# Performance work log

Measured on AMD Instinct MI355X. Metric: run time of the kernel, lower is better.

## Reference

```python
import jax, jax.numpy as jnp
import numpy as np

N, E = 16384, 262144
IN, H, OUT = 128, 256, 256
L, HEADS = 4, 8
OC = H // HEADS  # 32, also MHA head_dim
B, NB = 64, 256  # graphs, nodes per graph (N = B*NB, equal-size graphs)


def _ln(x, g, b, eps=1e-5):
    m = x.mean(-1, keepdims=True)
    v = ((x - m) ** 2).mean(-1, keepdims=True)
    return (x - m) / jnp.sqrt(v + eps) * g + b


def setup_inputs() -> dict:
    key = jax.random.key(0)
    ks = iter(jax.random.split(key, 40))
    r = lambda *s: jax.random.normal(next(ks), s, jnp.float32) * 0.05
    return dict(
        x=jax.random.normal(next(ks), (N, IN), jnp.float32),
        edge_index=jax.random.randint(next(ks), (2, E), 0, N),
        wi=r(IN, H), bi=r(H),
        wg=r(L, H, H), asrc=r(L, HEADS, OC), adst=r(L, HEADS, OC), bg=r(L, H),
        g1=jnp.ones((L, H)), b1=jnp.zeros((L, H)),
        inw=r(L, 3 * H, H), inb=r(L, 3 * H), ow=r(L, H, H), ob=r(L, H),
        g2=jnp.ones((L, H)), b2=jnp.zeros((L, H)),
        mw1=r(L, H, 2 * H), mb1=r(L, 2 * H), mw2=r(L, 2 * H, H), mb2=r(L, H),
        g3=jnp.ones((L, H)), b3=jnp.zeros((L, H)),
        gf=jnp.ones(H), bf=jnp.zeros(H),
        wo=r(H, OUT), bo=r(OUT),
    )


def reference(x, edge_index, wi, bi, wg, asrc, adst, bg, g1, b1, inw, inb,
              ow, ob, g2, b2, mw1, mb1, mw2, mb2, g3, b3, gf, bf, wo, bo):
    src, dst = edge_index[0], edge_index[1]
    x = jax.nn.relu(x @ wi + bi)  # [N, H]
    for i in range(L):
        # ---- GATConv (local MPNN), eval mode (no dropout) ----
        xw = (x @ wg[i]).reshape(N, HEADS, OC)
        a = (xw * asrc[i]).sum(-1)[src] + (xw * adst[i]).sum(-1)[dst]  # [E, HEADS]
        a = jax.nn.leaky_relu(a, 0.2)
        amax = jax.ops.segment_max(a, dst, num_segments=N)
        ae = jnp.exp(a - amax[dst])
        asum = jax.ops.segment_sum(ae, dst, num_segments=N)
        attn = ae / asum[dst]  # edge softmax per destination node
        h = jax.ops.segment_sum(attn[:, :, None] * xw[src], dst, num_segments=N)
        h = h.reshape(N, H) + bg[i]
        h = _ln(h + x, g1[i], b1[i])  # GPSConv local branch + residual + norm1
        # ---- global MultiheadAttention over dense batch (equal-size graphs) ----
        xd = x.reshape(B, NB, H)
        qkv = xd @ inw[i].T + inb[i]
        q, k, v = jnp.split(qkv, 3, axis=-1)
        q = q.reshape(B, NB, HEADS, OC).transpose(0, 2, 1, 3)
        k = k.reshape(B, NB, HEADS, OC).transpose(0, 2, 1, 3)
        v = v.reshape(B, NB, HEADS, OC).transpose(0, 2, 1, 3)
        p = jax.nn.softmax(jnp.einsum('bhqd,bhkd->bhqk', q, k) / jnp.sqrt(jnp.float32(OC)), axis=-1)
        o = jnp.einsum('bhqk,bhkd->bhqd', p, v).transpose(0, 2, 1, 3).reshape(B, NB, H)
        o = (o @ ow[i].T + ob[i]).reshape(N, H)
        h2 = _ln(o + x, g2[i], b2[i])  # global branch + residual + norm2
        out = h + h2
        out = out + (jax.nn.relu(out @ mw1[i] + mb1[i]) @ mw2[i] + mb2[i])  # MLP residual
        x = _ln(out, g3[i], b3[i])  # norm3
    x = _ln(x, gf, bf)
    return x @ wo + bo
```

## Files before the change

### kernel.cpp

```cpp
#include <hip/hip_runtime.h>
#include <hip/hip_bf16.h>

#define NNODES 16384
#define NEDGES 262144
#define IND    128
#define HD     256
#define OUTDIM 256
#define LAYERS 4
#define NHEADS 8
#define OCD    32
#define NGRAPH 64
#define NBATCH 256
#define XQSTR  1024

typedef __hip_bfloat16 bf16;
typedef __attribute__((ext_vector_type(8))) short bf16x8;
typedef __attribute__((ext_vector_type(4))) short s16x4;
typedef __attribute__((ext_vector_type(4))) float f32x4;

__device__ __forceinline__ short bfbits(float v) {
    bf16 h = __float2bfloat16(v);
    return *(short*)&h;
}
__device__ __forceinline__ float b2f(short s) {
    return __uint_as_float(((unsigned)(unsigned short)s) << 16);
}

__device__ __forceinline__ void gload_lds16(const short* g, short* l) {
    __builtin_amdgcn_global_load_lds(
        (const __attribute__((address_space(1))) void*)g,
        (__attribute__((address_space(3))) void*)l, 16, 0, 0);
}

#define PREP_TOTAL (32768 + NNODES*IND + IND*HD + LAYERS*1024*HD + LAYERS*1024 \
                    + LAYERS*HD*HD + LAYERS*HD*2*HD + LAYERS*2*HD*HD + HD*OUTDIM)
__global__ void prep_kernel(const float* __restrict__ x0, const float* __restrict__ wi,
                            const float* __restrict__ inw, const float* __restrict__ wg,
                            const float* __restrict__ inb, const float* __restrict__ ow,
                            const float* __restrict__ mw1, const float* __restrict__ mw2,
                            const float* __restrict__ wo,
                            short* __restrict__ x016, short* __restrict__ wi_t,
                            short* __restrict__ wcomb, float* __restrict__ cbias,
                            short* __restrict__ ow_c, short* __restrict__ mw1_t,
                            short* __restrict__ mw2_t, short* __restrict__ wo_t,
                            int* __restrict__ cnt, int* __restrict__ fill)
{
    int i = blockIdx.x * blockDim.x + threadIdx.x;
    if (i < 32768) {
        if (i < NNODES) cnt[i] = 0; else fill[i - NNODES] = 0;
        return;
    }
    i -= 32768;
    if (i < NNODES * IND) { x016[i] = bfbits(x0[i]); return; }
    i -= NNODES * IND;
    if (i < IND * HD) {
        int k = i / HD, n = i % HD;
        wi_t[n * IND + k] = bfbits(wi[i]);
        return;
    }
    i -= IND * HD;
    if (i < LAYERS * 1024 * HD) {
        int l = i >> 18, r = (i >> 8) & 1023, k = i & 255;
        float v = (r < 768) ? inw[(size_t)l * 768 * 256 + r * 256 + k]
                            : wg[(size_t)l * 256 * 256 + k * 256 + (r - 768)];
        wcomb[i] = bfbits(v);
        return;
    }
    i -= LAYERS * 1024 * HD;
    if (i < LAYERS * 1024) {
        int l = i >> 10, c = i & 1023;
        cbias[i] = (c < 768) ? inb[l * 768 + c] : 0.f;
        return;
    }
    i -= LAYERS * 1024;
    if (i < LAYERS * HD * HD) { ow_c[i] = bfbits(ow[i]); return; }
    i -= LAYERS * HD * HD;
    if (i < LAYERS * HD * 2 * HD) {
        int l = i / (HD * 2 * HD), r = i % (HD * 2 * HD);
        int k = r / (2 * HD), n = r % (2 * HD);
        mw1_t[(size_t)l * HD * 2 * HD + n * HD + k] = bfbits(mw1[i]);
        return;
    }
    i -= LAYERS * HD * 2 * HD;
    if (i < LAYERS * 2 * HD * HD) {
        int l = i / (2 * HD * HD), r = i % (2 * HD * HD);
        int k = r / HD, n = r % HD;
        mw2_t[(size_t)l * 2 * HD * HD + n * 2 * HD + k] = bfbits(mw2[i]);
        return;
    }
    i -= LAYERS * 2 * HD * HD;
    if (i < HD * OUTDIM) {
        int k = i / OUTDIM, n = i % OUTDIM;
        wo_t[n * HD + k] = bfbits(wo[i]);
    }
}

__global__ void hist_kernel(const int* __restrict__ dst, int* __restrict__ cnt)
{
    int e = blockIdx.x * blockDim.x + threadIdx.x;
    if (e < NEDGES) atomicAdd(&cnt[dst[e]], 1);
}

__global__ void scan_kernel(const int* __restrict__ cnt, int* __restrict__ row_ptr)
{
    __shared__ int part[256];
    int t = threadIdx.x;
    const int PER = NNODES / 256;
    int base = t * PER;
    int s = 0;
    for (int i = 0; i < PER; i++) s += cnt[base + i];
    part[t] = s;
    __syncthreads();
    for (int off = 1; off < 256; off <<= 1) {
        int v = (t >= off) ? part[t - off] : 0;
        __syncthreads();
        part[t] += v;
        __syncthreads();
    }
    int run = (t == 0) ? 0 : part[t - 1];
    for (int i = 0; i < PER; i++) { row_ptr[base + i] = run; run += cnt[base + i]; }
    if (t == 255) row_ptr[NNODES] = run;
}

__global__ void scatter_kernel(const int* __restrict__ src, const int* __restrict__ dst,
                               const int* __restrict__ row_ptr, int* __restrict__ fill,
                               int* __restrict__ srcs)
{
    int e = blockIdx.x * blockDim.x + threadIdx.x;
    if (e >= NEDGES) return;
    int d = dst[e];
    int pos = row_ptr[d] + atomicAdd(&fill[d], 1);
    srcs[pos] = src[e];
}

__global__ void gat_scores_kernel(const short* __restrict__ xw16,
                                  const float* __restrict__ asrc, const float* __restrict__ adst,
                                  float* __restrict__ ssrc, float* __restrict__ sdst)
{
    int i = blockIdx.x * blockDim.x + threadIdx.x;
    if (i >= NNODES * NHEADS) return;
    int n = i >> 3, h = i & 7;
    const bf16x8* xr = (const bf16x8*)(xw16 + (size_t)n * XQSTR + h * OCD);
    float s1 = 0.f, s2 = 0.f;
#pragma unroll
    for (int g = 0; g < 4; g++) {
        bf16x8 v8 = xr[g];
#pragma unroll
        for (int j = 0; j < 8; j++) {
            float v = b2f(v8[j]);
            int d = g * 8 + j;
            s1 += v * asrc[h * OCD + d];
            s2 += v * adst[h * OCD + d];
        }
    }
    ssrc[i] = s1;
    sdst[i] = s2;
}

__global__ __launch_bounds__(256)
void gat_agg_ln_kernel(const int* __restrict__ row_ptr, const int* __restrict__ srcs,
                       const float* __restrict__ ssrc, const float* __restrict__ sdst,
                       const short* __restrict__ xw16, const float* __restrict__ xcur,
                       const float* __restrict__ colbias, const float* __restrict__ gamma,
                       const float* __restrict__ beta, float* __restrict__ out)
{
    int wave = threadIdx.x >> 6, lane = threadIdx.x & 63;
    int n = blockIdx.x * 4 + wave;
    int c0 = lane << 2;
    int h = c0 >> 5;
    int start = row_ptr[n];
    int deg = row_ptr[n + 1] - start;
    float sd = sdst[n * NHEADS + h];

    float ax = 0.f, ay = 0.f, az = 0.f, aw = 0.f, l = 0.f;
    int j = 0;
    for (; j + 4 <= deg; j += 4) {
        int e0 = srcs[start + j + 0], e1 = srcs[start + j + 1];
        int e2 = srcs[start + j + 2], e3 = srcs[start + j + 3];
        s16x4 r0 = *(const s16x4*)&xw16[(size_t)e0 * XQSTR + c0];
        s16x4 r1 = *(const s16x4*)&xw16[(size_t)e1 * XQSTR + c0];
        s16x4 r2 = *(const s16x4*)&xw16[(size_t)e2 * XQSTR + c0];
        s16x4 r3 = *(const s16x4*)&xw16[(size_t)e3 * XQSTR + c0];
        float a0 = ssrc[e0 * NHEADS + h] + sd; a0 = a0 > 0.f ? a0 : 0.2f * a0;
        float a1 = ssrc[e1 * NHEADS + h] + sd; a1 = a1 > 0.f ? a1 : 0.2f * a1;
        float a2 = ssrc[e2 * NHEADS + h] + sd; a2 = a2 > 0.f ? a2 : 0.2f * a2;
        float a3 = ssrc[e3 * NHEADS + h] + sd; a3 = a3 > 0.f ? a3 : 0.2f * a3;
        float p0 = __expf(a0), p1 = __expf(a1), p2 = __expf(a2), p3 = __expf(a3);
        l += (p0 + p1) + (p2 + p3);
        ax += p0 * b2f(r0[0]) + p1 * b2f(r1[0]) + p2 * b2f(r2[0]) + p3 * b2f(r3[0]);
        ay += p0 * b2f(r0[1]) + p1 * b2f(r1[1]) + p2 * b2f(r2[1]) + p3 * b2f(r3[1]);
        az += p0 * b2f(r0[2]) + p1 * b2f(r1[2]) + p2 * b2f(r2[2]) + p3 * b2f(r3[2]);
        aw += p0 * b2f(r0[3]) + p1 * b2f(r1[3]) + p2 * b2f(r2[3]) + p3 * b2f(r3[3]);
    }
    for (; j < deg; j++) {
        int e0 = srcs[start + j];
        s16x4 r0 = *(const s16x4*)&xw16[(size_t)e0 * XQSTR + c0];
        float a0 = ssrc[e0 * NHEADS + h] + sd; a0 = a0 > 0.f ? a0 : 0.2f * a0;
        float p0 = __expf(a0);
        l += p0;
        ax += p0 * b2f(r0[0]); ay += p0 * b2f(r0[1]);
        az += p0 * b2f(r0[2]); aw += p0 * b2f(r0[3]);
    }
    float invl = deg ? 1.f / l : 0.f;
    size_t base = (size_t)n * HD + c0;
    float4 x4 = *(const float4*)&xcur[base];
    float4 cb = *(const float4*)&colbias[c0];
    float4 v;
    v.x = ax * invl + x4.x + cb.x;
    v.y = ay * invl + x4.y + cb.y;
    v.z = az * invl + x4.z + cb.z;
    v.w = aw * invl + x4.w + cb.w;
    float s = v.x + v.y + v.z + v.w;
    float q = v.x * v.x + v.y * v.y + v.z * v.z + v.w * v.w;
#pragma unroll
    for (int off = 1; off < 64; off <<= 1) {
        s += __shfl_xor(s, off);
        q += __shfl_xor(q, off);
    }
    float mean = s * (1.f / HD);
    float var  = fmaxf(q * (1.f / HD) - mean * mean, 0.f);
    float inv  = rsqrtf(var + 1e-5f);
    float4 g  = *(const float4*)&gamma[c0];
    float4 bt = *(const float4*)&beta[c0];
    float4 y;
    y.x = (v.x - mean) * inv * g.x + bt.x;
    y.y = (v.y - mean) * inv * g.y + bt.y;
    y.z = (v.z - mean) * inv * g.z + bt.z;
    y.w = (v.w - mean) * inv * g.w + bt.w;
    *(float4*)&out[base] = y;
}

#define GBM 128
#define GBK 32

template<int TN>
__global__ __launch_bounds__(256)
void gemm_mfma_kernel(const short* __restrict__ A16, const short* __restrict__ B16,
                      const float* __restrict__ bias, const float* __restrict__ resid,
                      float* __restrict__ Cf, short* __restrict__ C16,
                      int M, int Nc, int K, int relu)
{
    constexpr int NTF = TN / 32;
    __shared__ short As[GBM * GBK];
    __shared__ short Bs[TN * GBK];
    int tid = threadIdx.x;
    int wid = tid >> 6, lane = tid & 63;
    int quad = lane >> 4, l16 = lane & 15;
    int wm = wid >> 1, wn = wid & 1;
    int rowBase = blockIdx.y * GBM;
    int colBase = blockIdx.x * TN;

    f32x4 acc[4][NTF];
#pragma unroll
    for (int mt = 0; mt < 4; mt++)
#pragma unroll
        for (int nt = 0; nt < NTF; nt++) acc[mt][nt] = (f32x4)(0.f);

    const short* Ag0 = &A16[(size_t)(rowBase + lane) * K + wid * 8];
    const short* Ag1 = &A16[(size_t)(rowBase + 64 + lane) * K + wid * 8];
    const short* Bg0 = &B16[(size_t)(colBase + lane) * K + wid * 8];
    const short* Bg1 = (TN == 128) ? &B16[(size_t)(colBase + 64 + lane) * K + wid * 8] : nullptr;
    short* AsD0 = As + (wid * 128 + 0) * 8;
    short* AsD1 = As + (wid * 128 + 64) * 8;
    short* BsD0 = Bs + (wid * TN) * 8;
    short* BsD1 = Bs + (wid * TN + 64) * 8;

    for (int k0 = 0; k0 < K; k0 += GBK) {
        gload_lds16(Ag0 + k0, AsD0);
        gload_lds16(Ag1 + k0, AsD1);
        gload_lds16(Bg0 + k0, BsD0);
        if (TN == 128) gload_lds16(Bg1 + k0, BsD1);
        __syncthreads();
        bf16x8 aF[4], bF[NTF];
#pragma unroll
        for (int mt = 0; mt < 4; mt++)
            aF[mt] = *(bf16x8*)&As[(quad * 128 + wm * 64 + mt * 16 + l16) * 8];
#pragma unroll
        for (int nt = 0; nt < NTF; nt++)
            bF[nt] = *(bf16x8*)&Bs[(quad * TN + wn * (TN / 2) + nt * 16 + l16) * 8];
#pragma unroll
        for (int mt = 0; mt < 4; mt++)
#pragma unroll
            for (int nt = 0; nt < NTF; nt++)
                acc[mt][nt] = __builtin_amdgcn_mfma_f32_16x16x32_bf16(
                    bF[nt], aF[mt], acc[mt][nt], 0, 0, 0);
        __syncthreads();
    }

#pragma unroll
    for (int mt = 0; mt < 4; mt++) {
        int row = rowBase + wm * 64 + mt * 16 + l16;
#pragma unroll
        for (int nt = 0; nt < NTF; nt++) {
            int col0 = colBase + wn * (TN / 2) + nt * 16 + quad * 4;
            f32x4 v = acc[mt][nt];
            if (bias) {
                float4 b4 = *(const float4*)&bias[col0];
                v[0] += b4.x; v[1] += b4.y; v[2] += b4.z; v[3] += b4.w;
            }
            if (resid) {
                float4 r4 = *(const float4*)&resid[(size_t)row * Nc + col0];
                v[0] += r4.x; v[1] += r4.y; v[2] += r4.z; v[3] += r4.w;
            }
            if (relu) {
                v[0] = fmaxf(v[0], 0.f); v[1] = fmaxf(v[1], 0.f);
                v[2] = fmaxf(v[2], 0.f); v[3] = fmaxf(v[3], 0.f);
            }
            if (Cf) {
                float4 o; o.x = v[0]; o.y = v[1]; o.z = v[2]; o.w = v[3];
                *(float4*)&Cf[(size_t)row * Nc + col0] = o;
            }
            if (C16) {
                s16x4 o;
                o[0] = bfbits(v[0]); o[1] = bfbits(v[1]);
                o[2] = bfbits(v[2]); o[3] = bfbits(v[3]);
                *(s16x4*)&C16[(size_t)row * Nc + col0] = o;
            }
        }
    }
}

__global__ __launch_bounds__(256)
void gemm_ln_kernel(const short* __restrict__ A16, const short* __restrict__ B16,
                    const float* __restrict__ bias, const float* __restrict__ resid,
                    const float* __restrict__ gamma, const float* __restrict__ beta,
                    const float* __restrict__ postadd,
                    float* __restrict__ outf, short* __restrict__ out16, int K)
{
    __shared__ short As[64 * GBK];
    __shared__ short Bs[256 * GBK];
    int tid = threadIdx.x;
    int wid = tid >> 6, lane = tid & 63;
    int quad = lane >> 4, l16 = lane & 15;
    int rowBase = blockIdx.y * 64;

    f32x4 acc[16];
#pragma unroll
    for (int nt = 0; nt < 16; nt++) acc[nt] = (f32x4)(0.f);

    const short* Ag  = &A16[(size_t)(rowBase + lane) * K + wid * 8];
    const short* Bg0 = &B16[(size_t)(lane) * K + wid * 8];
    const short* Bg1 = &B16[(size_t)(64 + lane) * K + wid * 8];
    const short* Bg2 = &B16[(size_t)(128 + lane) * K + wid * 8];
    const short* Bg3 = &B16[(size_t)(192 + lane) * K + wid * 8];
    short* AsD  = As + (wid * 64) * 8;
    short* BsD0 = Bs + (wid * 256 + 0) * 8;
    short* BsD1 = Bs + (wid * 256 + 64) * 8;
    short* BsD2 = Bs + (wid * 256 + 128) * 8;
    short* BsD3 = Bs + (wid * 256 + 192) * 8;

    for (int k0 = 0; k0 < K; k0 += GBK) {
        gload_lds16(Ag + k0, AsD);
        gload_lds16(Bg0 + k0, BsD0);
        gload_lds16(Bg1 + k0, BsD1);
        gload_lds16(Bg2 + k0, BsD2);
        gload_lds16(Bg3 + k0, BsD3);
        __syncthreads();
        bf16x8 aF = *(bf16x8*)&As[(quad * 64 + wid * 16 + l16) * 8];
#pragma unroll
        for (int nt = 0; nt < 16; nt++) {
            bf16x8 bF = *(bf16x8*)&Bs[(quad * 256 + nt * 16 + l16) * 8];
            acc[nt] = __builtin_amdgcn_mfma_f32_16x16x32_bf16(bF, aF, acc[nt], 0, 0, 0);
        }
        __syncthreads();
    }

    int row = rowBase + wid * 16 + l16;
    float s = 0.f, q = 0.f;
#pragma unroll
    for (int nt = 0; nt < 16; nt++) {
        int col0 = nt * 16 + quad * 4;
        f32x4 v = acc[nt];
        float4 b4 = *(const float4*)&bias[col0];
        float4 r4 = *(const float4*)&resid[(size_t)row * HD + col0];
        v[0] += b4.x + r4.x; v[1] += b4.y + r4.y;
        v[2] += b4.z + r4.z; v[3] += b4.w + r4.w;
        acc[nt] = v;
        s += (v[0] + v[1]) + (v[2] + v[3]);
        q += (v[0] * v[0] + v[1] * v[1]) + (v[2] * v[2] + v[3] * v[3]);
    }
    s += __shfl_xor(s, 16); s += __shfl_xor(s, 32);
    q += __shfl_xor(q, 16); q += __shfl_xor(q, 32);
    float mean = s * (1.f / HD);
    float var  = fmaxf(q * (1.f / HD) - mean * mean, 0.f);
    float inv  = rsqrtf(var + 1e-5f);
#pragma unroll
    for (int nt = 0; nt < 16; nt++) {
        int col0 = nt * 16 + quad * 4;
        f32x4 v = acc[nt];
        float4 g4 = *(const float4*)&gamma[col0];
        float4 bt = *(const float4*)&beta[col0];
        float4 y;
        y.x = (v[0] - mean) * inv * g4.x + bt.x;
        y.y = (v[1] - mean) * inv * g4.y + bt.y;
        y.z = (v[2] - mean) * inv * g4.z + bt.z;
        y.w = (v[3] - mean) * inv * g4.w + bt.w;
        if (postadd) {
            float4 p4 = *(const float4*)&postadd[(size_t)row * HD + col0];
            y.x += p4.x; y.y += p4.y; y.z += p4.z; y.w += p4.w;
        }
        *(float4*)&outf[(size_t)row * HD + col0] = y;
        s16x4 o;
        o[0] = bfbits(y.x); o[1] = bfbits(y.y); o[2] = bfbits(y.z); o[3] = bfbits(y.w);
        *(s16x4*)&out16[(size_t)row * HD + col0] = o;
    }
}

__global__ __launch_bounds__(256)
void ln4_kernel(const float* __restrict__ in, const float* __restrict__ res,
                const float* __restrict__ gamma, const float* __restrict__ beta,
                const float* __restrict__ postadd,
                float* __restrict__ outf, short* __restrict__ out16)
{
    int wave = threadIdx.x >> 6, lane = threadIdx.x & 63;
    int row = blockIdx.x * 4 + wave;
    size_t base = (size_t)row * HD + lane * 4;
    float4 v = *(const float4*)&in[base];
    if (res) {
        float4 r = *(const float4*)&res[base];
        v.x += r.x; v.y += r.y; v.z += r.z; v.w += r.w;
    }
    float s = v.x + v.y + v.z + v.w;
    float q = v.x * v.x + v.y * v.y + v.z * v.z + v.w * v.w;
#pragma unroll
    for (int off = 1; off < 64; off <<= 1) {
        s += __shfl_xor(s, off);
        q += __shfl_xor(q, off);
    }
    float mean = s * (1.f / HD);
    float var  = fmaxf(q * (1.f / HD) - mean * mean, 0.f);
    float inv  = rsqrtf(var + 1e-5f);
    float4 g  = *(const float4*)&gamma[lane * 4];
    float4 bt = *(const float4*)&beta[lane * 4];
    float4 y;
    y.x = (v.x - mean) * inv * g.x + bt.x;
    y.y = (v.y - mean) * inv * g.y + bt.y;
    y.z = (v.z - mean) * inv * g.z + bt.z;
    y.w = (v.w - mean) * inv * g.w + bt.w;
    if (postadd) {
        float4 p = *(const float4*)&postadd[base];
        y.x += p.x; y.y += p.y; y.z += p.z; y.w += p.w;
    }
    if (outf) *(float4*)&outf[base] = y;
    if (out16) {
        s16x4 o;
        o[0] = bfbits(y.x); o[1] = bfbits(y.y); o[2] = bfbits(y.z); o[3] = bfbits(y.w);
        *(s16x4*)&out16[base] = o;
    }
}

#define PSTR 72
__global__ __launch_bounds__(256)
void mha_mfma_kernel(const short* __restrict__ qkv16, short* __restrict__ o16)
{
    __shared__ short smem[4 * 64 * PSTR + 32 * PSTR];
    short* VT = smem + 4 * 64 * PSTR;

    int b = blockIdx.x, h = blockIdx.y;
    int tid = threadIdx.x;
    int wid = tid >> 6, lane = tid & 63;
    int quad = lane >> 4, l16 = lane & 15;
    int base = b * NBATCH;
    int qrow0 = wid * 64;
    short* Pme = smem + wid * 64 * PSTR;

    const float scale2 = 0.17677669529663687f * 1.4426950408889634f;

    bf16x8 qA[4];
#pragma unroll
    for (int mt = 0; mt < 4; mt++)
        qA[mt] = *(const bf16x8*)&qkv16[(size_t)(base + qrow0 + mt * 16 + l16) * XQSTR + h * 32 + quad * 8];

    f32x4 accO[4][2];
#pragma unroll
    for (int mt = 0; mt < 4; mt++)
#pragma unroll
        for (int dt = 0; dt < 2; dt++) accO[mt][dt] = (f32x4)(0.f);
    float lsum[4][4];
#pragma unroll
    for (int mt = 0; mt < 4; mt++)
#pragma unroll
        for (int r = 0; r < 4; r++) lsum[mt][r] = 0.f;

    for (int c = 0; c < 4; c++) {
        __syncthreads();
        {
            int key = tid >> 2, dq = (tid & 3) * 8;
            bf16x8 v = *(const bf16x8*)&qkv16[(size_t)(base + c * 64 + key) * XQSTR + 512 + h * 32 + dq];
#pragma unroll
            for (int j = 0; j < 8; j++) VT[(dq + j) * PSTR + key] = v[j];
        }
        __syncthreads();
        bf16x8 kB[4];
#pragma unroll
        for (int kt = 0; kt < 4; kt++)
            kB[kt] = *(const bf16x8*)&qkv16[(size_t)(base + c * 64 + kt * 16 + l16) * XQSTR + 256 + h * 32 + quad * 8];
#pragma unroll
        for (int mt = 0; mt < 4; mt++) {
#pragma unroll
            for (int kt = 0; kt < 4; kt++) {
                f32x4 s = __builtin_amdgcn_mfma_f32_16x16x32_bf16(qA[mt], kB[kt], (f32x4)(0.f), 0, 0, 0);
#pragma unroll
                for (int r = 0; r < 4; r++) {
                    float p = exp2f(s[r] * scale2);
                    lsum[mt][r] += p;
                    Pme[(mt * 16 + quad * 4 + r) * PSTR + kt * 16 + l16] = bfbits(p);
                }
            }
        }
        __syncthreads();
#pragma unroll
        for (int mt = 0; mt < 4; mt++) {
#pragma unroll
            for (int ks = 0; ks < 2; ks++) {
                bf16x8 pA = *(bf16x8*)&Pme[(mt * 16 + l16) * PSTR + ks * 32 + quad * 8];
#pragma unroll
                for (int dt = 0; dt < 2; dt++) {
                    bf16x8 vB = *(bf16x8*)&VT[(dt * 16 + l16) * PSTR + ks * 32 + quad * 8];
                    accO[mt][dt] = __builtin_amdgcn_mfma_f32_16x16x32_bf16(pA, vB, accO[mt][dt], 0, 0, 0);
                }
            }
        }
    }
#pragma unroll
    for (int mt = 0; mt < 4; mt++)
#pragma unroll
        for (int r = 0; r < 4; r++) {
            float v = lsum[mt][r];
            v += __shfl_xor(v, 1);
            v += __shfl_xor(v, 2);
            v += __shfl_xor(v, 4);
            v += __shfl_xor(v, 8);
            lsum[mt][r] = v;
        }
#pragma unroll
    for (int mt = 0; mt < 4; mt++)
#pragma unroll
        for (int dt = 0; dt < 2; dt++)
#pragma unroll
            for (int r = 0; r < 4; r++) {
                int row = base + qrow0 + mt * 16 + quad * 4 + r;
                int col = h * 32 + dt * 16 + l16;
                o16[(size_t)row * HD + col] = bfbits(accO[mt][dt][r] / lsum[mt][r]);
            }
}

extern "C" void kernel_launch(void* const* d_in, const int* in_sizes, int n_in,
                              void* d_out, int out_size, void* d_ws, size_t ws_size,
                              hipStream_t stream)
{
    const float* x0   = (const float*)d_in[0];
    const int*   ei   = (const int*)d_in[1];
    const float* wi   = (const float*)d_in[2];
    const float* bi   = (const float*)d_in[3];
    const float* wg   = (const float*)d_in[4];
    const float* asrc = (const float*)d_in[5];
    const float* adst = (const float*)d_in[6];
    const float* bg   = (const float*)d_in[7];
    const float* g1   = (const float*)d_in[8];
    const float* b1   = (const float*)d_in[9];
    const float* inw  = (const float*)d_in[10];
    const float* inb  = (const float*)d_in[11];
    const float* ow   = (const float*)d_in[12];
    const float* ob   = (const float*)d_in[13];
    const float* g2   = (const float*)d_in[14];
    const float* b2   = (const float*)d_in[15];
    const float* mw1  = (const float*)d_in[16];
    const float* mb1  = (const float*)d_in[17];
    const float* mw2  = (const float*)d_in[18];
    const float* mb2  = (const float*)d_in[19];
    const float* g3   = (const float*)d_in[20];
    const float* b3   = (const float*)d_in[21];
    const float* gf   = (const float*)d_in[22];
    const float* bf_  = (const float*)d_in[23];
    const float* wo   = (const float*)d_in[24];
    const float* bo   = (const float*)d_in[25];

    const int* srcI = ei;
    const int* dstI = ei + NEDGES;

    const size_t NH = (size_t)NNODES * HD;
    float* ws   = (float*)d_ws;
    float* xcur = ws;
    float* xw   = xcur + NH;
    float* hbuf = xw + NH;
    float* obuf = hbuf + NH;
    float* qkvb = obuf + NH;
    int*   srcs    = (int*)(qkvb + 3 * NH);
    int*   row_ptr = srcs + NEDGES;
    int*   cnt     = row_ptr + NNODES + 1;
    int*   fill    = cnt + NNODES;
    float* ssrc    = (float*)(fill + NNODES);
    float* sdst    = ssrc + (size_t)NNODES * NHEADS;
    short* xq16   = (short*)qkvb;
    short* x016   = (short*)(sdst + (size_t)NNODES * NHEADS);
    short* xcur16 = x016 + (size_t)NNODES * IND;
    short* b16a   = xcur16 + NH;
    short* hid16  = b16a + NH;
    short* wi_t  = hid16 + 2 * NH;
    short* wcomb = wi_t + (size_t)HD * IND;
    short* ow_c  = wcomb + (size_t)LAYERS * 1024 * HD;
    short* mw1_t = ow_c + (size_t)LAYERS * HD * HD;
    short* mw2_t = mw1_t + (size_t)LAYERS * HD * 2 * HD;
    short* wo_t  = mw2_t + (size_t)LAYERS * 2 * HD * HD;
    float* cbias = (float*)(wo_t + (size_t)HD * OUTDIM);

    const int T = 256;
    const int nNH = NNODES * NHEADS;

    prep_kernel<<<(PREP_TOTAL + T - 1) / T, T, 0, stream>>>(
        x0, wi, inw, wg, inb, ow, mw1, mw2, wo,
        x016, wi_t, wcomb, cbias, ow_c, mw1_t, mw2_t, wo_t, cnt, fill);

    hist_kernel<<<(NEDGES + T - 1) / T, T, 0, stream>>>(dstI, cnt);
    scan_kernel<<<1, 256, 0, stream>>>(cnt, row_ptr);
    scatter_kernel<<<(NEDGES + T - 1) / T, T, 0, stream>>>(srcI, dstI, row_ptr, fill, srcs);

    gemm_mfma_kernel<64><<<dim3(HD / 64, NNODES / GBM), 256, 0, stream>>>(
        x016, wi_t, bi, nullptr, xcur, xcur16, NNODES, HD, IND, 1);

    for (int i = 0; i < LAYERS; i++) {
        const float* asrc_i = asrc + (size_t)i * NHEADS * OCD;
        const float* adst_i = adst + (size_t)i * NHEADS * OCD;
        const float* bg_i   = bg + (size_t)i * HD;
        const float* g1_i   = g1 + (size_t)i * HD;
        const float* b1_i   = b1 + (size_t)i * HD;
        const float* ob_i   = ob + (size_t)i * HD;
        const float* g2_i   = g2 + (size_t)i * HD;
        const float* b2_i   = b2 + (size_t)i * HD;
        const float* mb1_i  = mb1 + (size_t)i * 2 * HD;
        const float* mb2_i  = mb2 + (size_t)i * HD;
        const float* g3_i   = g3 + (size_t)i * HD;
        const float* b3_i   = b3 + (size_t)i * HD;
        const short* wcomb_i = wcomb + (size_t)i * 1024 * HD;
        const float* cbias_i = cbias + (size_t)i * 1024;
        const short* ow_ci  = ow_c + (size_t)i * HD * HD;
        const short* mw1_ti = mw1_t + (size_t)i * HD * 2 * HD;
        const short* mw2_ti = mw2_t + (size_t)i * 2 * HD * HD;

        gemm_mfma_kernel<128><<<dim3(1024 / 128, NNODES / GBM), 256, 0, stream>>>(
            xcur16, wcomb_i, cbias_i, nullptr, nullptr, xq16, NNODES, 1024, HD, 0);

        gat_scores_kernel<<<(nNH + T - 1) / T, T, 0, stream>>>(xq16 + 768, asrc_i, adst_i, ssrc, sdst);
        gat_agg_ln_kernel<<<NNODES / 4, 256, 0, stream>>>(
            row_ptr, srcs, ssrc, sdst, xq16 + 768, xcur, bg_i, g1_i, b1_i, hbuf);

        mha_mfma_kernel<<<dim3(NGRAPH, NHEADS), 256, 0, stream>>>(xq16, b16a);
        gemm_ln_kernel<<<dim3(1, NNODES / 64), 256, 0, stream>>>(
            b16a, ow_ci, ob_i, xcur, g2_i, b2_i, hbuf, obuf, b16a, HD);

        gemm_mfma_kernel<128><<<dim3(2 * HD / 128, NNODES / GBM), 256, 0, stream>>>(
            b16a, mw1_ti, mb1_i, nullptr, nullptr, hid16, NNODES, 2 * HD, HD, 1);
        gemm_ln_kernel<<<dim3(1, NNODES / 64), 256, 0, stream>>>(
            hid16, mw2_ti, mb2_i, obuf, g3_i, b3_i, nullptr, xcur, xcur16, 2 * HD);
    }

    ln4_kernel<<<NNODES / 4, 256, 0, stream>>>(xcur, nullptr, gf, bf_, nullptr, nullptr, b16a);
    gemm_mfma_kernel<64><<<dim3(OUTDIM / 64, NNODES / GBM), 256, 0, stream>>>(
        b16a, wo_t, bo, nullptr, (float*)d_out, nullptr, NNODES, OUTDIM, HD, 0);
}
```

Before: 843.7 us.

## Store bf16 activations and weights in 64x8 blocked tile layout

```diff
diff --git a/kernel.cpp b/kernel.cpp
--- a/kernel.cpp
+++ b/kernel.cpp
@@ -11,7 +11,6 @@
 #define OCD    32
 #define NGRAPH 64
 #define NBATCH 256
-#define XQSTR  1024
 
 typedef __hip_bfloat16 bf16;
 typedef __attribute__((ext_vector_type(8))) short bf16x8;
@@ -24,6 +23,10 @@
 }
 __device__ __forceinline__ float b2f(short s) {
     return __uint_as_float(((unsigned)(unsigned short)s) << 16);
+}
+
+__device__ __forceinline__ size_t bidx(int row, int col, int KC) {
+    return ((size_t)((row >> 6) * KC + (col >> 3)) << 9) + ((row & 63) << 3) + (col & 7);
 }
 
 __device__ __forceinline__ void gload_lds16(const short* g, short* l) {
@@ -51,11 +54,15 @@
         return;
     }
     i -= 32768;
-    if (i < NNODES * IND) { x016[i] = bfbits(x0[i]); return; }
+    if (i < NNODES * IND) {
+        int row = i / IND, col = i % IND;
+        x016[bidx(row, col, 16)] = bfbits(x0[i]);
+        return;
+    }
     i -= NNODES * IND;
     if (i < IND * HD) {
         int k = i / HD, n = i % HD;
-        wi_t[n * IND + k] = bfbits(wi[i]);
+        wi_t[bidx(n, k, 16)] = bfbits(wi[i]);
         return;
     }
     i -= IND * HD;
@@ -63,7 +70,7 @@
         int l = i >> 18, r = (i >> 8) & 1023, k = i & 255;
         float v = (r < 768) ? inw[(size_t)l * 768 * 256 + r * 256 + k]
                             : wg[(size_t)l * 256 * 256 + k * 256 + (r - 768)];
-        wcomb[i] = bfbits(v);
+        wcomb[((size_t)l << 18) + bidx(r, k, 32)] = bfbits(v);
         return;
     }
     i -= LAYERS * 1024 * HD;
@@ -73,25 +80,29 @@
         return;
     }
     i -= LAYERS * 1024;
-    if (i < LAYERS * HD * HD) { ow_c[i] = bfbits(ow[i]); return; }
+    if (i < LAYERS * HD * HD) {
+        int l = i >> 16, rem = i & 65535, r = rem >> 8, k = rem & 255;
+        ow_c[((size_t)l << 16) + bidx(r, k, 32)] = bfbits(ow[i]);
+        return;
+    }
     i -= LAYERS * HD * HD;
     if (i < LAYERS * HD * 2 * HD) {
-        int l = i / (HD * 2 * HD), r = i % (HD * 2 * HD);
-        int k = r / (2 * HD), n = r % (2 * HD);
-        mw1_t[(size_t)l * HD * 2 * HD + n * HD + k] = bfbits(mw1[i]);
+        int l = i / (HD * 2 * HD), rem = i % (HD * 2 * HD);
+        int k = rem / (2 * HD), n = rem % (2 * HD);
+        mw1_t[(size_t)l * HD * 2 * HD + bidx(n, k, 32)] = bfbits(mw1[i]);
         return;
     }
     i -= LAYERS * HD * 2 * HD;
     if (i < LAYERS * 2 * HD * HD) {
-        int l = i / (2 * HD * HD), r = i % (2 * HD * HD);
-        int k = r / HD, n = r % HD;
-        mw2_t[(size_t)l * 2 * HD * HD + n * 2 * HD + k] = bfbits(mw2[i]);
+        int l = i / (2 * HD * HD), rem = i % (2 * HD * HD);
+        int k = rem / HD, n = rem % HD;
+        mw2_t[(size_t)l * 2 * HD * HD + bidx(n, k, 64)] = bfbits(mw2[i]);
         return;
     }
     i -= LAYERS * 2 * HD * HD;
     if (i < HD * OUTDIM) {
         int k = i / OUTDIM, n = i % OUTDIM;
-        wo_t[n * HD + k] = bfbits(wo[i]);
+        wo_t[bidx(n, k, 32)] = bfbits(wo[i]);
     }
 }
 
@@ -133,18 +144,17 @@
     srcs[pos] = src[e];
 }
 
-__global__ void gat_scores_kernel(const short* __restrict__ xw16,
+__global__ void gat_scores_kernel(const short* __restrict__ xq16,
                                   const float* __restrict__ asrc, const float* __restrict__ adst,
                                   float* __restrict__ ssrc, float* __restrict__ sdst)
 {
     int i = blockIdx.x * blockDim.x + threadIdx.x;
     if (i >= NNODES * NHEADS) return;
     int n = i >> 3, h = i & 7;
-    const bf16x8* xr = (const bf16x8*)(xw16 + (size_t)n * XQSTR + h * OCD);
     float s1 = 0.f, s2 = 0.f;
 #pragma unroll
     for (int g = 0; g < 4; g++) {
-        bf16x8 v8 = xr[g];
+        bf16x8 v8 = *(const bf16x8*)&xq16[bidx(n, 768 + h * OCD + g * 8, 128)];
 #pragma unroll
         for (int j = 0; j < 8; j++) {
             float v = b2f(v8[j]);
@@ -160,7 +170,7 @@
 __global__ __launch_bounds__(256)
 void gat_agg_ln_kernel(const int* __restrict__ row_ptr, const int* __restrict__ srcs,
                        const float* __restrict__ ssrc, const float* __restrict__ sdst,
-                       const short* __restrict__ xw16, const float* __restrict__ xcur,
+                       const short* __restrict__ xq16, const float* __restrict__ xcur,
                        const float* __restrict__ colbias, const float* __restrict__ gamma,
                        const float* __restrict__ beta, float* __restrict__ out)
 {
@@ -177,10 +187,10 @@
     for (; j + 4 <= deg; j += 4) {
         int e0 = srcs[start + j + 0], e1 = srcs[start + j + 1];
         int e2 = srcs[start + j + 2], e3 = srcs[start + j + 3];
-        s16x4 r0 = *(const s16x4*)&xw16[(size_t)e0 * XQSTR + c0];
-        s16x4 r1 = *(const s16x4*)&xw16[(size_t)e1 * XQSTR + c0];
-        s16x4 r2 = *(const s16x4*)&xw16[(size_t)e2 * XQSTR + c0];
-        s16x4 r3 = *(const s16x4*)&xw16[(size_t)e3 * XQSTR + c0];
+        s16x4 r0 = *(const s16x4*)&xq16[bidx(e0, 768 + c0, 128)];
+        s16x4 r1 = *(const s16x4*)&xq16[bidx(e1, 768 + c0, 128)];
+        s16x4 r2 = *(const s16x4*)&xq16[bidx(e2, 768 + c0, 128)];
+        s16x4 r3 = *(const s16x4*)&xq16[bidx(e3, 768 + c0, 128)];
         float a0 = ssrc[e0 * NHEADS + h] + sd; a0 = a0 > 0.f ? a0 : 0.2f * a0;
         float a1 = ssrc[e1 * NHEADS + h] + sd; a1 = a1 > 0.f ? a1 : 0.2f * a1;
         float a2 = ssrc[e2 * NHEADS + h] + sd; a2 = a2 > 0.f ? a2 : 0.2f * a2;
@@ -194,7 +204,7 @@
     }
     for (; j < deg; j++) {
         int e0 = srcs[start + j];
-        s16x4 r0 = *(const s16x4*)&xw16[(size_t)e0 * XQSTR + c0];
+        s16x4 r0 = *(const s16x4*)&xq16[bidx(e0, 768 + c0, 128)];
         float a0 = ssrc[e0 * NHEADS + h] + sd; a0 = a0 > 0.f ? a0 : 0.2f * a0;
         float p0 = __expf(a0);
         l += p0;
@@ -249,6 +259,7 @@
     int wm = wid >> 1, wn = wid & 1;
     int rowBase = blockIdx.y * GBM;
     int colBase = blockIdx.x * TN;
+    int KC = K >> 3;
 
     f32x4 acc[4][NTF];
 #pragma unroll
@@ -256,20 +267,21 @@
 #pragma unroll
         for (int nt = 0; nt < NTF; nt++) acc[mt][nt] = (f32x4)(0.f);
 
-    const short* Ag0 = &A16[(size_t)(rowBase + lane) * K + wid * 8];
-    const short* Ag1 = &A16[(size_t)(rowBase + 64 + lane) * K + wid * 8];
-    const short* Bg0 = &B16[(size_t)(colBase + lane) * K + wid * 8];
-    const short* Bg1 = (TN == 128) ? &B16[(size_t)(colBase + 64 + lane) * K + wid * 8] : nullptr;
+    const short* Ag0 = A16 + (((size_t)(blockIdx.y * 2 + 0) * KC + wid) << 9) + lane * 8;
+    const short* Ag1 = A16 + (((size_t)(blockIdx.y * 2 + 1) * KC + wid) << 9) + lane * 8;
+    const short* Bg0 = B16 + (((size_t)((colBase >> 6) + 0) * KC + wid) << 9) + lane * 8;
+    const short* Bg1 = (TN == 128) ?
+        B16 + (((size_t)((colBase >> 6) + 1) * KC + wid) << 9) + lane * 8 : nullptr;
     short* AsD0 = As + (wid * 128 + 0) * 8;
     short* AsD1 = As + (wid * 128 + 64) * 8;
     short* BsD0 = Bs + (wid * TN) * 8;
     short* BsD1 = Bs + (wid * TN + 64) * 8;
 
-    for (int k0 = 0; k0 < K; k0 += GBK) {
-        gload_lds16(Ag0 + k0, AsD0);
-        gload_lds16(Ag1 + k0, AsD1);
-        gload_lds16(Bg0 + k0, BsD0);
-        if (TN == 128) gload_lds16(Bg1 + k0, BsD1);
+    for (int t = 0; t < (K >> 5); t++) {
+        gload_lds16(Ag0 + t * 2048, AsD0);
+        gload_lds16(Ag1 + t * 2048, AsD1);
+        gload_lds16(Bg0 + t * 2048, BsD0);
+        if (TN == 128) gload_lds16(Bg1 + t * 2048, BsD1);
         __syncthreads();
         bf16x8 aF[4], bF[NTF];
 #pragma unroll
@@ -314,7 +326,7 @@
                 s16x4 o;
                 o[0] = bfbits(v[0]); o[1] = bfbits(v[1]);
                 o[2] = bfbits(v[2]); o[3] = bfbits(v[3]);
-                *(s16x4*)&C16[(size_t)row * Nc + col0] = o;
+                *(s16x4*)&C16[bidx(row, col0, Nc >> 3)] = o;
             }
         }
     }
@@ -333,28 +345,29 @@
     int wid = tid >> 6, lane = tid & 63;
     int quad = lane >> 4, l16 = lane & 15;
     int rowBase = blockIdx.y * 64;
+    int KC = K >> 3;
 
     f32x4 acc[16];
 #pragma unroll
     for (int nt = 0; nt < 16; nt++) acc[nt] = (f32x4)(0.f);
 
-    const short* Ag  = &A16[(size_t)(rowBase + lane) * K + wid * 8];
-    const short* Bg0 = &B16[(size_t)(lane) * K + wid * 8];
-    const short* Bg1 = &B16[(size_t)(64 + lane) * K + wid * 8];
-    const short* Bg2 = &B16[(size_t)(128 + lane) * K + wid * 8];
-    const short* Bg3 = &B16[(size_t)(192 + lane) * K + wid * 8];
+    const short* Ag  = A16 + (((size_t)blockIdx.y * KC + wid) << 9) + lane * 8;
+    const short* Bg0 = B16 + (((size_t)0 * KC + wid) << 9) + lane * 8;
+    const short* Bg1 = B16 + (((size_t)1 * KC + wid) << 9) + lane * 8;
+    const short* Bg2 = B16 + (((size_t)2 * KC + wid) << 9) + lane * 8;
+    const short* Bg3 = B16 + (((size_t)3 * KC + wid) << 9) + lane * 8;
     short* AsD  = As + (wid * 64) * 8;
     short* BsD0 = Bs + (wid * 256 + 0) * 8;
     short* BsD1 = Bs + (wid * 256 + 64) * 8;
     short* BsD2 = Bs + (wid * 256 + 128) * 8;
     short* BsD3 = Bs + (wid * 256 + 192) * 8;
 
-    for (int k0 = 0; k0 < K; k0 += GBK) {
-        gload_lds16(Ag + k0, AsD);
-        gload_lds16(Bg0 + k0, BsD0);
-        gload_lds16(Bg1 + k0, BsD1);
-        gload_lds16(Bg2 + k0, BsD2);
-        gload_lds16(Bg3 + k0, BsD3);
+    for (int t = 0; t < (K >> 5); t++) {
+        gload_lds16(Ag + t * 2048, AsD);
+        gload_lds16(Bg0 + t * 2048, BsD0);
+        gload_lds16(Bg1 + t * 2048, BsD1);
+        gload_lds16(Bg2 + t * 2048, BsD2);
+        gload_lds16(Bg3 + t * 2048, BsD3);
         __syncthreads();
         bf16x8 aF = *(bf16x8*)&As[(quad * 64 + wid * 16 + l16) * 8];
 #pragma unroll
@@ -402,7 +415,7 @@
         *(float4*)&outf[(size_t)row * HD + col0] = y;
         s16x4 o;
         o[0] = bfbits(y.x); o[1] = bfbits(y.y); o[2] = bfbits(y.z); o[3] = bfbits(y.w);
-        *(s16x4*)&out16[(size_t)row * HD + col0] = o;
+        *(s16x4*)&out16[bidx(row, col0, 32)] = o;
     }
 }
 
@@ -445,7 +458,7 @@
     if (out16) {
         s16x4 o;
         o[0] = bfbits(y.x); o[1] = bfbits(y.y); o[2] = bfbits(y.z); o[3] = bfbits(y.w);
-        *(s16x4*)&out16[base] = o;
+        *(s16x4*)&out16[bidx(row, lane * 4, 32)] = o;
     }
 }
 
@@ -469,7 +482,7 @@
     bf16x8 qA[4];
 #pragma unroll
     for (int mt = 0; mt < 4; mt++)
-        qA[mt] = *(const bf16x8*)&qkv16[(size_t)(base + qrow0 + mt * 16 + l16) * XQSTR + h * 32 + quad * 8];
+        qA[mt] = *(const bf16x8*)&qkv16[bidx(base + qrow0 + mt * 16 + l16, h * 32 + quad * 8, 128)];
 
     f32x4 accO[4][2];
 #pragma unroll
@@ -486,7 +499,7 @@
         __syncthreads();
         {
             int key = tid >> 2, dq = (tid & 3) * 8;
-            bf16x8 v = *(const bf16x8*)&qkv16[(size_t)(base + c * 64 + key) * XQSTR + 512 + h * 32 + dq];
+            bf16x8 v = *(const bf16x8*)&qkv16[bidx(base + c * 64 + key, 512 + h * 32 + dq, 128)];
 #pragma unroll
             for (int j = 0; j < 8; j++) VT[(dq + j) * PSTR + key] = v[j];
         }
@@ -494,7 +507,7 @@
         bf16x8 kB[4];
 #pragma unroll
         for (int kt = 0; kt < 4; kt++)
-            kB[kt] = *(const bf16x8*)&qkv16[(size_t)(base + c * 64 + kt * 16 + l16) * XQSTR + 256 + h * 32 + quad * 8];
+            kB[kt] = *(const bf16x8*)&qkv16[bidx(base + c * 64 + kt * 16 + l16, 256 + h * 32 + quad * 8, 128)];
 #pragma unroll
         for (int mt = 0; mt < 4; mt++) {
 #pragma unroll
@@ -541,7 +554,7 @@
             for (int r = 0; r < 4; r++) {
                 int row = base + qrow0 + mt * 16 + quad * 4 + r;
                 int col = h * 32 + dt * 16 + l16;
-                o16[(size_t)row * HD + col] = bfbits(accO[mt][dt][r] / lsum[mt][r]);
+                o16[bidx(row, col, 32)] = bfbits(accO[mt][dt][r] / lsum[mt][r]);
             }
 }
 
@@ -641,9 +654,9 @@
         gemm_mfma_kernel<128><<<dim3(1024 / 128, NNODES / GBM), 256, 0, stream>>>(
             xcur16, wcomb_i, cbias_i, nullptr, nullptr, xq16, NNODES, 1024, HD, 0);
 
-        gat_scores_kernel<<<(nNH + T - 1) / T, T, 0, stream>>>(xq16 + 768, asrc_i, adst_i, ssrc, sdst);
+        gat_scores_kernel<<<(nNH + T - 1) / T, T, 0, stream>>>(xq16, asrc_i, adst_i, ssrc, sdst);
         gat_agg_ln_kernel<<<NNODES / 4, 256, 0, stream>>>(
-            row_ptr, srcs, ssrc, sdst, xq16 + 768, xcur, bg_i, g1_i, b1_i, hbuf);
+            row_ptr, srcs, ssrc, sdst, xq16, xcur, bg_i, g1_i, b1_i, hbuf);
 
         mha_mfma_kernel<<<dim3(NGRAPH, NHEADS), 256, 0, stream>>>(xq16, b16a);
         gemm_ln_kernel<<<dim3(1, NNODES / 64), 256, 0, stream>>>(
```

Result: slower. 1.003 ms (+18.9%).
